# Kernel optimization log

Hardware: AMD Instinct MI355X
Metric: run time of the kernel (lower is better)

The kernel has to match this reference:

```python
import jax, jax.numpy as jnp
import numpy as np

N_NODES = 50000
N_EDGES = 625000
D_FEAT = 128


def setup_inputs() -> dict:
    key = jax.random.key(0)
    k1, k2, k3, k4 = jax.random.split(key, 4)
    h = jax.random.normal(k1, (N_NODES, D_FEAT), dtype=jnp.float32)
    w = jax.random.uniform(k2, (N_EDGES, 1), dtype=jnp.float32)
    src = jax.random.randint(k3, (N_EDGES,), 0, N_NODES, dtype=jnp.int32)
    dst = jax.random.randint(k4, (N_EDGES,), 0, N_NODES, dtype=jnp.int32)
    return {"h": h, "w": w, "src": src, "dst": dst, "mode": 1}


def reference(h, w, src, dst, mode):
    # h: [N, D] node features; w: [E, 1] edge weights; src/dst: [E] edge list.
    n = h.shape[0]
    if mode == 1:  # 'polar': m = h[src] * w, sum to dst  (edge-weighted SpMM)
        msg = h[src] * w  # [E, D]
        out = jax.ops.segment_sum(msg, dst, num_segments=n)
    else:  # GCN symmetric normalization: D^{-1/2} A D^{-1/2} h (out-degree based)
        deg = jax.ops.segment_sum(jnp.ones(src.shape[0], dtype=h.dtype), src,
                                  num_segments=n)
        norm = jnp.power(deg, -0.5)[:, None]  # [N, 1]
        feat = h * norm
        out = jax.ops.segment_sum(feat[src], dst, num_segments=n)
        out = norm * out
    return out
```

## Files before the change

kernel.cpp:

```cpp
#include <hip/hip_runtime.h>
#include <hip/hip_fp16.h>

#define D_FEAT 128


__device__ __forceinline__ unsigned wq16(float f) {
    int q = (int)(f * 65536.0f);
    if (q < 0) q = 0;
    if (q > 65535) q = 65535;
    return (unsigned)q;
}

__device__ __forceinline__ unsigned h2u(__half2 v) {
    union { __half2 h; unsigned u; } cv; cv.h = v; return cv.u;
}
__device__ __forceinline__ float2 u2f2(unsigned u) {
    union { unsigned u; __half2 h; } cv; cv.u = u;
    return __half22float2(cv.h);
}

__global__ void bucket_conv_kernel(const float* __restrict__ h,
                                   const int* __restrict__ src, const int* __restrict__ dst,
                                   const float* __restrict__ w,
                                   int* __restrict__ cursor, float* __restrict__ deg,
                                   int* __restrict__ ovfcnt, int* __restrict__ ovf,
                                   unsigned* __restrict__ rec, int cap,
                                   uint4* __restrict__ h16,
                                   int E, int nBucketBlocks, int nGroups8, int cs,
                                   const int* __restrict__ mode) {
    if ((int)blockIdx.x >= nBucketBlocks) {
        int i = (blockIdx.x - nBucketBlocks) * blockDim.x + threadIdx.x;
        if (i >= nGroups8) return;
        const float4* hf4 = (const float4*)h;
        float4 x = hf4[2 * i];
        float4 y = hf4[2 * i + 1];
        uint4 o;
        o.x = h2u(__float22half2_rn(make_float2(x.x, x.y)));
        o.y = h2u(__float22half2_rn(make_float2(x.z, x.w)));
        o.z = h2u(__float22half2_rn(make_float2(y.x, y.y)));
        o.w = h2u(__float22half2_rn(make_float2(y.z, y.w)));
        h16[i] = o;
        return;
    }
    int e = blockIdx.x * blockDim.x + threadIdx.x;
    if (e >= E) return;
    bool m1 = (*mode == 1);
    int s = src[e];
    int d = dst[e];
    float wv = w[e];
    if (!m1) atomicAdd(&deg[s], 1.0f);
    int pos = atomicAdd(&cursor[(size_t)d * cs], 1);
    unsigned r = ((unsigned)s << 16) | wq16(wv);
    if (pos < cap) rec[(size_t)d * cap + pos] = r;
    else           ovf[atomicAdd(ovfcnt, 1)] = e;
}

__device__ __forceinline__ unsigned bcast_rec(unsigned r0, unsigned r1, int j) {
    unsigned lo = __shfl(r0, j & 31, 32);
    unsigned hi = __shfl(r1, j & 31, 32);
    return (j < 32) ? lo : hi;
}

__global__ void gather4_f16_kernel(const uint2* __restrict__ h16,
                                   const float* __restrict__ hf,
                                   const int* __restrict__ cursor, const float* __restrict__ deg,
                                   const unsigned* __restrict__ rec, int cap,
                                   const int* __restrict__ ovfcnt, const int* __restrict__ ovf,
                                   const int* __restrict__ src, const int* __restrict__ dst,
                                   const float* __restrict__ w,
                                   float* __restrict__ out, int N, int cs,
                                   const int* __restrict__ mode) {
    long long gid = (long long)blockIdx.x * blockDim.x + threadIdx.x;
    int node = (int)(gid >> 5);
    int lane = (int)(gid & 31);
    if (node >= N) return;
    bool m1 = (*mode == 1);
    int cnt = cursor[(size_t)node * cs];
    int inb = cnt < cap ? cnt : cap;
    const unsigned* row = rec + (size_t)node * cap;
    unsigned r0 = (lane < inb) ? row[lane] : 0u;
    unsigned r1 = (lane + 32 < inb) ? row[lane + 32] : 0u;

    float a0 = 0.f, a1 = 0.f, a2 = 0.f, a3 = 0.f;
    float b0 = 0.f, b1 = 0.f, b2 = 0.f, b3 = 0.f;
    float c0 = 0.f, c1 = 0.f, c2 = 0.f, c3 = 0.f;
    float d0 = 0.f, d1 = 0.f, d2 = 0.f, d3 = 0.f;

    int j = 0;
    if (m1) {
        const float Q = 1.52587890625e-05f;
        for (; j + 7 < inb; j += 8) {
            unsigned m0 = bcast_rec(r0, r1, j);
            unsigned m1r = bcast_rec(r0, r1, j + 1);
            unsigned m2r = bcast_rec(r0, r1, j + 2);
            unsigned m3r = bcast_rec(r0, r1, j + 3);
            unsigned m4r = bcast_rec(r0, r1, j + 4);
            unsigned m5r = bcast_rec(r0, r1, j + 5);
            unsigned m6r = bcast_rec(r0, r1, j + 6);
            unsigned m7r = bcast_rec(r0, r1, j + 7);
            uint2 v0 = h16[(size_t)(m0 >> 16) * 32 + lane];
            uint2 v1 = h16[(size_t)(m1r >> 16) * 32 + lane];
            uint2 v2 = h16[(size_t)(m2r >> 16) * 32 + lane];
            uint2 v3 = h16[(size_t)(m3r >> 16) * 32 + lane];
            uint2 v4 = h16[(size_t)(m4r >> 16) * 32 + lane];
            uint2 v5 = h16[(size_t)(m5r >> 16) * 32 + lane];
            uint2 v6 = h16[(size_t)(m6r >> 16) * 32 + lane];
            uint2 v7 = h16[(size_t)(m7r >> 16) * 32 + lane];
            float sc0 = ((float)(m0 & 0xFFFFu) + 0.5f) * Q;
            float sc1 = ((float)(m1r & 0xFFFFu) + 0.5f) * Q;
            float sc2 = ((float)(m2r & 0xFFFFu) + 0.5f) * Q;
            float sc3 = ((float)(m3r & 0xFFFFu) + 0.5f) * Q;
            float sc4 = ((float)(m4r & 0xFFFFu) + 0.5f) * Q;
            float sc5 = ((float)(m5r & 0xFFFFu) + 0.5f) * Q;
            float sc6 = ((float)(m6r & 0xFFFFu) + 0.5f) * Q;
            float sc7 = ((float)(m7r & 0xFFFFu) + 0.5f) * Q;
            float2 f0a = u2f2(v0.x), f0b = u2f2(v0.y);
            float2 f1a = u2f2(v1.x), f1b = u2f2(v1.y);
            float2 f2a = u2f2(v2.x), f2b = u2f2(v2.y);
            float2 f3a = u2f2(v3.x), f3b = u2f2(v3.y);
            float2 f4a = u2f2(v4.x), f4b = u2f2(v4.y);
            float2 f5a = u2f2(v5.x), f5b = u2f2(v5.y);
            float2 f6a = u2f2(v6.x), f6b = u2f2(v6.y);
            float2 f7a = u2f2(v7.x), f7b = u2f2(v7.y);
            a0 += f0a.x * sc0; a1 += f0a.y * sc0; a2 += f0b.x * sc0; a3 += f0b.y * sc0;
            b0 += f1a.x * sc1; b1 += f1a.y * sc1; b2 += f1b.x * sc1; b3 += f1b.y * sc1;
            c0 += f2a.x * sc2; c1 += f2a.y * sc2; c2 += f2b.x * sc2; c3 += f2b.y * sc2;
            d0 += f3a.x * sc3; d1 += f3a.y * sc3; d2 += f3b.x * sc3; d3 += f3b.y * sc3;
            a0 += f4a.x * sc4; a1 += f4a.y * sc4; a2 += f4b.x * sc4; a3 += f4b.y * sc4;
            b0 += f5a.x * sc5; b1 += f5a.y * sc5; b2 += f5b.x * sc5; b3 += f5b.y * sc5;
            c0 += f6a.x * sc6; c1 += f6a.y * sc6; c2 += f6b.x * sc6; c3 += f6b.y * sc6;
            d0 += f7a.x * sc7; d1 += f7a.y * sc7; d2 += f7b.x * sc7; d3 += f7b.y * sc7;
        }
        for (; j + 3 < inb; j += 4) {
            unsigned m0 = bcast_rec(r0, r1, j);
            unsigned m1r = bcast_rec(r0, r1, j + 1);
            unsigned m2r = bcast_rec(r0, r1, j + 2);
            unsigned m3r = bcast_rec(r0, r1, j + 3);
            float sc0 = ((float)(m0 & 0xFFFFu) + 0.5f) * Q;
            float sc1 = ((float)(m1r & 0xFFFFu) + 0.5f) * Q;
            float sc2 = ((float)(m2r & 0xFFFFu) + 0.5f) * Q;
            float sc3 = ((float)(m3r & 0xFFFFu) + 0.5f) * Q;
            uint2 v0 = h16[(size_t)(m0 >> 16) * 32 + lane];
            uint2 v1 = h16[(size_t)(m1r >> 16) * 32 + lane];
            uint2 v2 = h16[(size_t)(m2r >> 16) * 32 + lane];
            uint2 v3 = h16[(size_t)(m3r >> 16) * 32 + lane];
            float2 f0a = u2f2(v0.x), f0b = u2f2(v0.y);
            float2 f1a = u2f2(v1.x), f1b = u2f2(v1.y);
            float2 f2a = u2f2(v2.x), f2b = u2f2(v2.y);
            float2 f3a = u2f2(v3.x), f3b = u2f2(v3.y);
            a0 += f0a.x * sc0; a1 += f0a.y * sc0; a2 += f0b.x * sc0; a3 += f0b.y * sc0;
            b0 += f1a.x * sc1; b1 += f1a.y * sc1; b2 += f1b.x * sc1; b3 += f1b.y * sc1;
            c0 += f2a.x * sc2; c1 += f2a.y * sc2; c2 += f2b.x * sc2; c3 += f2b.y * sc2;
            d0 += f3a.x * sc3; d1 += f3a.y * sc3; d2 += f3b.x * sc3; d3 += f3b.y * sc3;
        }
        for (; j < inb; ++j) {
            unsigned m0 = bcast_rec(r0, r1, j);
            float sc0 = ((float)(m0 & 0xFFFFu) + 0.5f) * Q;
            uint2 v0 = h16[(size_t)(m0 >> 16) * 32 + lane];
            float2 f0a = u2f2(v0.x), f0b = u2f2(v0.y);
            a0 += f0a.x * sc0; a1 += f0a.y * sc0; a2 += f0b.x * sc0; a3 += f0b.y * sc0;
        }
    } else {
        for (; j + 3 < inb; j += 4) {
            unsigned m0 = bcast_rec(r0, r1, j);
            unsigned m1r = bcast_rec(r0, r1, j + 1);
            unsigned m2r = bcast_rec(r0, r1, j + 2);
            unsigned m3r = bcast_rec(r0, r1, j + 3);
            int s0 = (int)(m0 >> 16), s1 = (int)(m1r >> 16);
            int s2 = (int)(m2r >> 16), s3 = (int)(m3r >> 16);
            float sc0 = rsqrtf(deg[s0]);
            float sc1 = rsqrtf(deg[s1]);
            float sc2 = rsqrtf(deg[s2]);
            float sc3 = rsqrtf(deg[s3]);
            uint2 v0 = h16[(size_t)s0 * 32 + lane];
            uint2 v1 = h16[(size_t)s1 * 32 + lane];
            uint2 v2 = h16[(size_t)s2 * 32 + lane];
            uint2 v3 = h16[(size_t)s3 * 32 + lane];
            float2 f0a = u2f2(v0.x), f0b = u2f2(v0.y);
            float2 f1a = u2f2(v1.x), f1b = u2f2(v1.y);
            float2 f2a = u2f2(v2.x), f2b = u2f2(v2.y);
            float2 f3a = u2f2(v3.x), f3b = u2f2(v3.y);
            a0 += f0a.x * sc0; a1 += f0a.y * sc0; a2 += f0b.x * sc0; a3 += f0b.y * sc0;
            b0 += f1a.x * sc1; b1 += f1a.y * sc1; b2 += f1b.x * sc1; b3 += f1b.y * sc1;
            c0 += f2a.x * sc2; c1 += f2a.y * sc2; c2 += f2b.x * sc2; c3 += f2b.y * sc2;
            d0 += f3a.x * sc3; d1 += f3a.y * sc3; d2 += f3b.x * sc3; d3 += f3b.y * sc3;
        }
        for (; j < inb; ++j) {
            unsigned m0 = bcast_rec(r0, r1, j);
            int s0 = (int)(m0 >> 16);
            float sc0 = rsqrtf(deg[s0]);
            uint2 v0 = h16[(size_t)s0 * 32 + lane];
            float2 f0a = u2f2(v0.x), f0b = u2f2(v0.y);
            a0 += f0a.x * sc0; a1 += f0a.y * sc0; a2 += f0b.x * sc0; a3 += f0b.y * sc0;
        }
    }

    a0 += b0 + c0 + d0; a1 += b1 + c1 + d1;
    a2 += b2 + c2 + d2; a3 += b3 + c3 + d3;

    if (cnt > cap) {
        int total = *ovfcnt;
        for (int k = 0; k < total; ++k) {
            int e = ovf[k];
            if (dst[e] == node) {
                int s = src[e];
                float sc = m1 ? w[e] : rsqrtf(deg[s]);
                float4 v = ((const float4*)(hf + (long long)s * D_FEAT))[lane];
                a0 += v.x * sc; a1 += v.y * sc; a2 += v.z * sc; a3 += v.w * sc;
            }
        }
    }
    float fin = m1 ? 1.0f : rsqrtf(deg[node]);
    float4 r; r.x = a0 * fin; r.y = a1 * fin; r.z = a2 * fin; r.w = a3 * fin;
    ((float4*)(out + (long long)node * D_FEAT))[lane] = r;
}


__global__ void bucket_multi_kernel(const int* __restrict__ src, const int* __restrict__ dst,
                                    const float* __restrict__ w,
                                    int* __restrict__ cursor, float* __restrict__ deg,
                                    int* __restrict__ ovfcnt, int* __restrict__ ovf,
                                    unsigned* __restrict__ rec, int cap,
                                    int E, const int* __restrict__ mode) {
    int e = blockIdx.x * blockDim.x + threadIdx.x;
    if (e >= E) return;
    bool m1 = (*mode == 1);
    int s = src[e], d = dst[e];
    if (!m1) atomicAdd(&deg[s], 1.0f);
    int pos = atomicAdd(&cursor[d], 1);
    if (pos < cap) rec[(size_t)d * cap + pos] = ((unsigned)s << 16) | wq16(w[e]);
    else ovf[atomicAdd(ovfcnt, 1)] = e;
}

__global__ void gather4_f32_kernel(const float* __restrict__ h,
                                   const int* __restrict__ cursor, const float* __restrict__ deg,
                                   const unsigned* __restrict__ rec, int cap,
                                   const int* __restrict__ ovfcnt, const int* __restrict__ ovf,
                                   const int* __restrict__ src, const int* __restrict__ dst,
                                   const float* __restrict__ w,
                                   float* __restrict__ out, int N, const int* __restrict__ mode) {
    long long gid = (long long)blockIdx.x * blockDim.x + threadIdx.x;
    int node = (int)(gid >> 5);
    int lane = (int)(gid & 31);
    if (node >= N) return;
    bool m1 = (*mode == 1);
    int cnt = cursor[node];
    int inb = cnt < cap ? cnt : cap;
    const unsigned* row = rec + (size_t)node * cap;
    unsigned r0 = (lane < inb) ? row[lane] : 0u;
    unsigned r1 = (lane + 32 < inb) ? row[lane + 32] : 0u;
    const float4* h4 = (const float4*)h;
    float a0 = 0.f, a1 = 0.f, a2 = 0.f, a3 = 0.f;
    float b0 = 0.f, b1 = 0.f, b2 = 0.f, b3 = 0.f;
    int j = 0;
    const float Q = 1.52587890625e-05f;
    for (; j + 1 < inb; j += 2) {
        unsigned m0 = bcast_rec(r0, r1, j);
        unsigned m1r = bcast_rec(r0, r1, j + 1);
        int s0 = (int)(m0 >> 16), s1 = (int)(m1r >> 16);
        float sc0 = m1 ? ((float)(m0 & 0xFFFFu) + 0.5f) * Q : rsqrtf(deg[s0]);
        float sc1 = m1 ? ((float)(m1r & 0xFFFFu) + 0.5f) * Q : rsqrtf(deg[s1]);
        float4 v0 = h4[(size_t)s0 * 32 + lane];
        float4 v1 = h4[(size_t)s1 * 32 + lane];
        a0 += v0.x * sc0; a1 += v0.y * sc0; a2 += v0.z * sc0; a3 += v0.w * sc0;
        b0 += v1.x * sc1; b1 += v1.y * sc1; b2 += v1.z * sc1; b3 += v1.w * sc1;
    }
    if (j < inb) {
        unsigned m0 = bcast_rec(r0, r1, j);
        int s0 = (int)(m0 >> 16);
        float sc0 = m1 ? ((float)(m0 & 0xFFFFu) + 0.5f) * Q : rsqrtf(deg[s0]);
        float4 v0 = h4[(size_t)s0 * 32 + lane];
        a0 += v0.x * sc0; a1 += v0.y * sc0; a2 += v0.z * sc0; a3 += v0.w * sc0;
    }
    a0 += b0; a1 += b1; a2 += b2; a3 += b3;
    if (cnt > cap) {
        int total = *ovfcnt;
        for (int k = 0; k < total; ++k) {
            int e = ovf[k];
            if (dst[e] == node) {
                int s = src[e];
                float sc = m1 ? w[e] : rsqrtf(deg[s]);
                float4 v = ((const float4*)(h + (long long)s * D_FEAT))[lane];
                a0 += v.x * sc; a1 += v.y * sc; a2 += v.z * sc; a3 += v.w * sc;
            }
        }
    }
    float fin = m1 ? 1.0f : rsqrtf(deg[node]);
    float4 r; r.x = a0 * fin; r.y = a1 * fin; r.z = a2 * fin; r.w = a3 * fin;
    ((float4*)(out + (long long)node * D_FEAT))[lane] = r;
}


__global__ void fb_deg_kernel(const int* __restrict__ src, float* __restrict__ deg,
                              int E, const int* __restrict__ mode) {
    if (*mode == 1) return;
    int e = blockIdx.x * blockDim.x + threadIdx.x;
    if (e < E) atomicAdd(&deg[src[e]], 1.0f);
}
__global__ void fb_norm_kernel(const float* __restrict__ deg, float* __restrict__ norm,
                               int N, const int* __restrict__ mode) {
    if (*mode == 1) return;
    int i = blockIdx.x * blockDim.x + threadIdx.x;
    if (i < N) norm[i] = rsqrtf(deg[i]);
}
__global__ void fb_scatter_kernel(const float* __restrict__ h, const float* __restrict__ w,
                                  const int* __restrict__ src, const int* __restrict__ dst,
                                  const float* __restrict__ norm, float* __restrict__ out,
                                  int E, const int* __restrict__ mode) {
    long long gid = (long long)blockIdx.x * blockDim.x + threadIdx.x;
    int e = (int)(gid >> 5);
    int lane = (int)(gid & 31);
    if (e >= E) return;
    int s = src[e], d = dst[e];
    float scale = (*mode == 1) ? w[e] : norm[s];
    float4 v = ((const float4*)(h + (long long)s * D_FEAT))[lane];
    float* op = out + (long long)d * D_FEAT + lane * 4;
    atomicAdd(op + 0, v.x * scale);
    atomicAdd(op + 1, v.y * scale);
    atomicAdd(op + 2, v.z * scale);
    atomicAdd(op + 3, v.w * scale);
}
__global__ void fb_scale_kernel(float* __restrict__ out, const float* __restrict__ norm,
                                int N, const int* __restrict__ mode) {
    if (*mode == 1) return;
    int idx = blockIdx.x * blockDim.x + threadIdx.x;
    int total = N * (D_FEAT / 4);
    if (idx >= total) return;
    int node = idx / (D_FEAT / 4);
    float4* op = (float4*)out + idx;
    float4 v = *op;
    float nn = norm[node];
    v.x *= nn; v.y *= nn; v.z *= nn; v.w *= nn;
    *op = v;
}


extern "C" void kernel_launch(void* const* d_in, const int* in_sizes, int n_in,
                              void* d_out, int out_size, void* d_ws, size_t ws_size,
                              hipStream_t stream) {
    const float* h    = (const float*)d_in[0];
    const float* w    = (const float*)d_in[1];
    const int*   src  = (const int*)d_in[2];
    const int*   dst  = (const int*)d_in[3];
    const int*   mode = (const int*)d_in[4];

    int ND = in_sizes[0];
    int E  = in_sizes[1];
    int N  = ND / D_FEAT;

    float* out = (float*)d_out;

    size_t ws_words = ws_size / 4;

    for (int cs : {16, 4, 1}) {
        size_t cur_words   = (size_t)N * cs;
        size_t fixed_words = cur_words + (size_t)N + 1 + (size_t)E;
        size_t h16_off     = (fixed_words + 3) & ~(size_t)3;
        size_t h16_words   = (size_t)N * (D_FEAT / 2);
        size_t rec16_off   = h16_off + h16_words;
        long capH = 0;
        if (ws_words > rec16_off) capH = (long)((ws_words - rec16_off) / (size_t)N);
        if (capH > 64) capH = 64;

        if (N <= 65536 && capH >= 28) {
            int*      cursor = (int*)d_ws;
            float*    deg    = (float*)(cursor + cur_words);
            int*      ovfcnt = (int*)(deg + N);
            int*      ovf    = ovfcnt + 1;
            uint4*    h16    = (uint4*)((int*)d_ws + h16_off);
            unsigned* rec    = (unsigned*)((int*)d_ws + rec16_off);
            int cap = (int)capH;
            int csv = cs;
            size_t zero_words = cur_words + (size_t)N + 1;

            hipMemsetAsync(d_ws, 0, zero_words * sizeof(int), stream);

            int nGroups8    = ND / 8;
            int nBucketBlks = (E + 255) / 256;
            int nConvBlks   = (nGroups8 + 255) / 256;
            bucket_conv_kernel<<<nBucketBlks + nConvBlks, 256, 0, stream>>>(
                h, src, dst, w, cursor, deg, ovfcnt, ovf, rec, cap, h16,
                E, nBucketBlks, nGroups8, csv, mode);

            long long gt = (long long)N * 32;
            gather4_f16_kernel<<<(int)((gt + 255) / 256), 256, 0, stream>>>(
                (const uint2*)h16, h, cursor, deg, rec, cap, ovfcnt, ovf, src, dst, w,
                out, N, csv, mode);
            return;
        }
    }

    size_t fixed_words = 2 * (size_t)N + 1 + (size_t)E;
    int*   cursor = (int*)d_ws;
    float* deg    = (float*)(cursor + N);
    int*   ovfcnt = (int*)(deg + N);
    int*   ovf    = ovfcnt + 1;

    size_t rec_off = fixed_words;
    long capA = 0;
    if (ws_words > rec_off) capA = (long)((ws_words - rec_off) / (size_t)N);
    if (capA > 64) capA = 64;

    if (N <= 65536 && capA >= 28) {
        unsigned* rec = (unsigned*)((int*)d_ws + rec_off);
        int cap = (int)capA;
        hipMemsetAsync(d_ws, 0, (2 * (size_t)N + 1) * sizeof(int), stream);
        bucket_multi_kernel<<<(E + 255) / 256, 256, 0, stream>>>(
            src, dst, w, cursor, deg, ovfcnt, ovf, rec, cap, E, mode);
        long long gt = (long long)N * 32;
        gather4_f32_kernel<<<(int)((gt + 255) / 256), 256, 0, stream>>>(
            h, cursor, deg, rec, cap, ovfcnt, ovf, src, dst, w, out, N, mode);
        return;
    }

    float* degF  = (float*)d_ws;
    float* normF = degF + N;
    hipMemsetAsync(d_out, 0, (size_t)out_size * sizeof(float), stream);
    hipMemsetAsync(d_ws, 0, (size_t)N * sizeof(float), stream);
    fb_deg_kernel<<<(E + 255) / 256, 256, 0, stream>>>(src, degF, E, mode);
    fb_norm_kernel<<<(N + 255) / 256, 256, 0, stream>>>(degF, normF, N, mode);
    long long tt = (long long)E * 32;
    fb_scatter_kernel<<<(int)((tt + 255) / 256), 256, 0, stream>>>(h, w, src, dst,
                                                                   normF, out, E, mode);
    int st = N * (D_FEAT / 4);
    fb_scale_kernel<<<(st + 255) / 256, 256, 0, stream>>>(out, normF, N, mode);
}
```

Before: 154.1 us.

## Split per-node bucket cursor into four sub-cursors to cut atomic contention

The bucketing step now spreads each destination's atomic cursor across four padded sub-counters, chosen by edge index mod 4, each owning a quarter of the record capacity. The gather kernel reads the four counts and maps a flat edge index to a segment position with a small branchy helper. The aim is to reduce same-address atomic contention during bucketing. In exchange it adds a larger zeroed cursor region (64 words per node), per-edge index arithmetic in the gather loop, loss of the 8-wide unrolled loop, and a higher chance of overflow because each quarter bucket can fill on its own.

```diff
diff --git a/kernel.cpp b/kernel.cpp
--- a/kernel.cpp
+++ b/kernel.cpp
@@ -24,9 +24,9 @@
                                    const float* __restrict__ w,
                                    int* __restrict__ cursor, float* __restrict__ deg,
                                    int* __restrict__ ovfcnt, int* __restrict__ ovf,
-                                   unsigned* __restrict__ rec, int cap,
+                                   unsigned* __restrict__ rec, int cap, int capq,
                                    uint4* __restrict__ h16,
-                                   int E, int nBucketBlocks, int nGroups8, int cs,
+                                   int E, int nBucketBlocks, int nGroups8,
                                    const int* __restrict__ mode) {
     if ((int)blockIdx.x >= nBucketBlocks) {
         int i = (blockIdx.x - nBucketBlocks) * blockDim.x + threadIdx.x;
@@ -49,10 +49,11 @@
     int d = dst[e];
     float wv = w[e];
     if (!m1) atomicAdd(&deg[s], 1.0f);
-    int pos = atomicAdd(&cursor[(size_t)d * cs], 1);
+    int kq = e & 3;
+    int pos = atomicAdd(&cursor[(size_t)d * 64 + kq * 16], 1);
     unsigned r = ((unsigned)s << 16) | wq16(wv);
-    if (pos < cap) rec[(size_t)d * cap + pos] = r;
-    else           ovf[atomicAdd(ovfcnt, 1)] = e;
+    if (pos < capq) rec[(size_t)d * cap + kq * capq + pos] = r;
+    else            ovf[atomicAdd(ovfcnt, 1)] = e;
 }
 
 __device__ __forceinline__ unsigned bcast_rec(unsigned r0, unsigned r1, int j) {
@@ -61,81 +62,61 @@
     return (j < 32) ? lo : hi;
 }
 
+__device__ __forceinline__ int segidx(int t, int c0, int c1, int c2, int capq) {
+    if (t < c0) return t;
+    t -= c0;
+    if (t < c1) return capq + t;
+    t -= c1;
+    if (t < c2) return 2 * capq + t;
+    t -= c2;
+    return 3 * capq + t;
+}
+
 __global__ void gather4_f16_kernel(const uint2* __restrict__ h16,
                                    const float* __restrict__ hf,
                                    const int* __restrict__ cursor, const float* __restrict__ deg,
-                                   const unsigned* __restrict__ rec, int cap,
+                                   const unsigned* __restrict__ rec, int cap, int capq,
                                    const int* __restrict__ ovfcnt, const int* __restrict__ ovf,
                                    const int* __restrict__ src, const int* __restrict__ dst,
                                    const float* __restrict__ w,
-                                   float* __restrict__ out, int N, int cs,
+                                   float* __restrict__ out, int N,
                                    const int* __restrict__ mode) {
     long long gid = (long long)blockIdx.x * blockDim.x + threadIdx.x;
     int node = (int)(gid >> 5);
     int lane = (int)(gid & 31);
     if (node >= N) return;
     bool m1 = (*mode == 1);
-    int cnt = cursor[(size_t)node * cs];
-    int inb = cnt < cap ? cnt : cap;
+
+    const int* cbase = cursor + (size_t)node * 64;
+    int n0 = cbase[0], n1 = cbase[16], n2 = cbase[32], n3 = cbase[48];
+    int c0 = n0 < capq ? n0 : capq;
+    int c1 = n1 < capq ? n1 : capq;
+    int c2 = n2 < capq ? n2 : capq;
+    int c3 = n3 < capq ? n3 : capq;
+    int total = c0 + c1 + c2 + c3;
+    bool ovfl = (n0 > capq) | (n1 > capq) | (n2 > capq) | (n3 > capq);
+
     const unsigned* row = rec + (size_t)node * cap;
-    unsigned r0 = (lane < inb) ? row[lane] : 0u;
-    unsigned r1 = (lane + 32 < inb) ? row[lane + 32] : 0u;
+    unsigned r0 = (lane < cap) ? row[lane] : 0u;
+    unsigned r1 = (lane + 32 < cap) ? row[lane + 32] : 0u;
 
     float a0 = 0.f, a1 = 0.f, a2 = 0.f, a3 = 0.f;
     float b0 = 0.f, b1 = 0.f, b2 = 0.f, b3 = 0.f;
-    float c0 = 0.f, c1 = 0.f, c2 = 0.f, c3 = 0.f;
+    float e0 = 0.f, e1 = 0.f, e2 = 0.f, e3 = 0.f;
     float d0 = 0.f, d1 = 0.f, d2 = 0.f, d3 = 0.f;
 
-    int j = 0;
+    int t = 0;
     if (m1) {
         const float Q = 1.52587890625e-05f;
-        for (; j + 7 < inb; j += 8) {
-            unsigned m0 = bcast_rec(r0, r1, j);
-            unsigned m1r = bcast_rec(r0, r1, j + 1);
-            unsigned m2r = bcast_rec(r0, r1, j + 2);
-            unsigned m3r = bcast_rec(r0, r1, j + 3);
-            unsigned m4r = bcast_rec(r0, r1, j + 4);
-            unsigned m5r = bcast_rec(r0, r1, j + 5);
-            unsigned m6r = bcast_rec(r0, r1, j + 6);
-            unsigned m7r = bcast_rec(r0, r1, j + 7);
-            uint2 v0 = h16[(size_t)(m0 >> 16) * 32 + lane];
-            uint2 v1 = h16[(size_t)(m1r >> 16) * 32 + lane];
-            uint2 v2 = h16[(size_t)(m2r >> 16) * 32 + lane];
-            uint2 v3 = h16[(size_t)(m3r >> 16) * 32 + lane];
-            uint2 v4 = h16[(size_t)(m4r >> 16) * 32 + lane];
-            uint2 v5 = h16[(size_t)(m5r >> 16) * 32 + lane];
-            uint2 v6 = h16[(size_t)(m6r >> 16) * 32 + lane];
-            uint2 v7 = h16[(size_t)(m7r >> 16) * 32 + lane];
-            float sc0 = ((float)(m0 & 0xFFFFu) + 0.5f) * Q;
-            float sc1 = ((float)(m1r & 0xFFFFu) + 0.5f) * Q;
-            float sc2 = ((float)(m2r & 0xFFFFu) + 0.5f) * Q;
-            float sc3 = ((float)(m3r & 0xFFFFu) + 0.5f) * Q;
-            float sc4 = ((float)(m4r & 0xFFFFu) + 0.5f) * Q;
-            float sc5 = ((float)(m5r & 0xFFFFu) + 0.5f) * Q;
-            float sc6 = ((float)(m6r & 0xFFFFu) + 0.5f) * Q;
-            float sc7 = ((float)(m7r & 0xFFFFu) + 0.5f) * Q;
-            float2 f0a = u2f2(v0.x), f0b = u2f2(v0.y);
-            float2 f1a = u2f2(v1.x), f1b = u2f2(v1.y);
-            float2 f2a = u2f2(v2.x), f2b = u2f2(v2.y);
-            float2 f3a = u2f2(v3.x), f3b = u2f2(v3.y);
-            float2 f4a = u2f2(v4.x), f4b = u2f2(v4.y);
-            float2 f5a = u2f2(v5.x), f5b = u2f2(v5.y);
-            float2 f6a = u2f2(v6.x), f6b = u2f2(v6.y);
-            float2 f7a = u2f2(v7.x), f7b = u2f2(v7.y);
-            a0 += f0a.x * sc0; a1 += f0a.y * sc0; a2 += f0b.x * sc0; a3 += f0b.y * sc0;
-            b0 += f1a.x * sc1; b1 += f1a.y * sc1; b2 += f1b.x * sc1; b3 += f1b.y * sc1;
-            c0 += f2a.x * sc2; c1 += f2a.y * sc2; c2 += f2b.x * sc2; c3 += f2b.y * sc2;
-            d0 += f3a.x * sc3; d1 += f3a.y * sc3; d2 += f3b.x * sc3; d3 += f3b.y * sc3;
-            a0 += f4a.x * sc4; a1 += f4a.y * sc4; a2 += f4b.x * sc4; a3 += f4b.y * sc4;
-            b0 += f5a.x * sc5; b1 += f5a.y * sc5; b2 += f5b.x * sc5; b3 += f5b.y * sc5;
-            c0 += f6a.x * sc6; c1 += f6a.y * sc6; c2 += f6b.x * sc6; c3 += f6b.y * sc6;
-            d0 += f7a.x * sc7; d1 += f7a.y * sc7; d2 += f7b.x * sc7; d3 += f7b.y * sc7;
-        }
-        for (; j + 3 < inb; j += 4) {
-            unsigned m0 = bcast_rec(r0, r1, j);
-            unsigned m1r = bcast_rec(r0, r1, j + 1);
-            unsigned m2r = bcast_rec(r0, r1, j + 2);
-            unsigned m3r = bcast_rec(r0, r1, j + 3);
+        for (; t + 3 < total; t += 4) {
+            int i0 = segidx(t,     c0, c1, c2, capq);
+            int i1 = segidx(t + 1, c0, c1, c2, capq);
+            int i2 = segidx(t + 2, c0, c1, c2, capq);
+            int i3 = segidx(t + 3, c0, c1, c2, capq);
+            unsigned m0 = bcast_rec(r0, r1, i0);
+            unsigned m1r = bcast_rec(r0, r1, i1);
+            unsigned m2r = bcast_rec(r0, r1, i2);
+            unsigned m3r = bcast_rec(r0, r1, i3);
             float sc0 = ((float)(m0 & 0xFFFFu) + 0.5f) * Q;
             float sc1 = ((float)(m1r & 0xFFFFu) + 0.5f) * Q;
             float sc2 = ((float)(m2r & 0xFFFFu) + 0.5f) * Q;
@@ -150,22 +131,27 @@
             float2 f3a = u2f2(v3.x), f3b = u2f2(v3.y);
             a0 += f0a.x * sc0; a1 += f0a.y * sc0; a2 += f0b.x * sc0; a3 += f0b.y * sc0;
             b0 += f1a.x * sc1; b1 += f1a.y * sc1; b2 += f1b.x * sc1; b3 += f1b.y * sc1;
-            c0 += f2a.x * sc2; c1 += f2a.y * sc2; c2 += f2b.x * sc2; c3 += f2b.y * sc2;
+            e0 += f2a.x * sc2; e1 += f2a.y * sc2; e2 += f2b.x * sc2; e3 += f2b.y * sc2;
             d0 += f3a.x * sc3; d1 += f3a.y * sc3; d2 += f3b.x * sc3; d3 += f3b.y * sc3;
         }
-        for (; j < inb; ++j) {
-            unsigned m0 = bcast_rec(r0, r1, j);
+        for (; t < total; ++t) {
+            int i0 = segidx(t, c0, c1, c2, capq);
+            unsigned m0 = bcast_rec(r0, r1, i0);
             float sc0 = ((float)(m0 & 0xFFFFu) + 0.5f) * Q;
             uint2 v0 = h16[(size_t)(m0 >> 16) * 32 + lane];
             float2 f0a = u2f2(v0.x), f0b = u2f2(v0.y);
             a0 += f0a.x * sc0; a1 += f0a.y * sc0; a2 += f0b.x * sc0; a3 += f0b.y * sc0;
         }
     } else {
-        for (; j + 3 < inb; j += 4) {
-            unsigned m0 = bcast_rec(r0, r1, j);
-            unsigned m1r = bcast_rec(r0, r1, j + 1);
-            unsigned m2r = bcast_rec(r0, r1, j + 2);
-            unsigned m3r = bcast_rec(r0, r1, j + 3);
+        for (; t + 3 < total; t += 4) {
+            int i0 = segidx(t,     c0, c1, c2, capq);
+            int i1 = segidx(t + 1, c0, c1, c2, capq);
+            int i2 = segidx(t + 2, c0, c1, c2, capq);
+            int i3 = segidx(t + 3, c0, c1, c2, capq);
+            unsigned m0 = bcast_rec(r0, r1, i0);
+            unsigned m1r = bcast_rec(r0, r1, i1);
+            unsigned m2r = bcast_rec(r0, r1, i2);
+            unsigned m3r = bcast_rec(r0, r1, i3);
             int s0 = (int)(m0 >> 16), s1 = (int)(m1r >> 16);
             int s2 = (int)(m2r >> 16), s3 = (int)(m3r >> 16);
             float sc0 = rsqrtf(deg[s0]);
@@ -182,11 +168,12 @@
             float2 f3a = u2f2(v3.x), f3b = u2f2(v3.y);
             a0 += f0a.x * sc0; a1 += f0a.y * sc0; a2 += f0b.x * sc0; a3 += f0b.y * sc0;
             b0 += f1a.x * sc1; b1 += f1a.y * sc1; b2 += f1b.x * sc1; b3 += f1b.y * sc1;
-            c0 += f2a.x * sc2; c1 += f2a.y * sc2; c2 += f2b.x * sc2; c3 += f2b.y * sc2;
+            e0 += f2a.x * sc2; e1 += f2a.y * sc2; e2 += f2b.x * sc2; e3 += f2b.y * sc2;
             d0 += f3a.x * sc3; d1 += f3a.y * sc3; d2 += f3b.x * sc3; d3 += f3b.y * sc3;
         }
-        for (; j < inb; ++j) {
-            unsigned m0 = bcast_rec(r0, r1, j);
+        for (; t < total; ++t) {
+            int i0 = segidx(t, c0, c1, c2, capq);
+            unsigned m0 = bcast_rec(r0, r1, i0);
             int s0 = (int)(m0 >> 16);
             float sc0 = rsqrtf(deg[s0]);
             uint2 v0 = h16[(size_t)s0 * 32 + lane];
@@ -195,12 +182,12 @@
         }
     }
 
-    a0 += b0 + c0 + d0; a1 += b1 + c1 + d1;
-    a2 += b2 + c2 + d2; a3 += b3 + c3 + d3;
-
-    if (cnt > cap) {
-        int total = *ovfcnt;
-        for (int k = 0; k < total; ++k) {
+    a0 += b0 + e0 + d0; a1 += b1 + e1 + d1;
+    a2 += b2 + e2 + d2; a3 += b3 + e3 + d3;
+
+    if (ovfl) {
+        int tot = *ovfcnt;
+        for (int k = 0; k < tot; ++k) {
             int e = ovf[k];
             if (dst[e] == node) {
                 int s = src[e];
@@ -352,8 +339,8 @@
 
     size_t ws_words = ws_size / 4;
 
-    for (int cs : {16, 4, 1}) {
-        size_t cur_words   = (size_t)N * cs;
+    {
+        size_t cur_words   = (size_t)N * 64;
         size_t fixed_words = cur_words + (size_t)N + 1 + (size_t)E;
         size_t h16_off     = (fixed_words + 3) & ~(size_t)3;
         size_t h16_words   = (size_t)N * (D_FEAT / 2);
@@ -361,16 +348,17 @@
         long capH = 0;
         if (ws_words > rec16_off) capH = (long)((ws_words - rec16_off) / (size_t)N);
         if (capH > 64) capH = 64;
-
-        if (N <= 65536 && capH >= 28) {
+        capH &= ~3L;
+
+        if (N <= 65536 && capH >= 32) {
             int*      cursor = (int*)d_ws;
             float*    deg    = (float*)(cursor + cur_words);
             int*      ovfcnt = (int*)(deg + N);
             int*      ovf    = ovfcnt + 1;
             uint4*    h16    = (uint4*)((int*)d_ws + h16_off);
             unsigned* rec    = (unsigned*)((int*)d_ws + rec16_off);
-            int cap = (int)capH;
-            int csv = cs;
+            int cap  = (int)capH;
+            int capq = cap / 4;
             size_t zero_words = cur_words + (size_t)N + 1;
 
             hipMemsetAsync(d_ws, 0, zero_words * sizeof(int), stream);
@@ -379,13 +367,13 @@
             int nBucketBlks = (E + 255) / 256;
             int nConvBlks   = (nGroups8 + 255) / 256;
             bucket_conv_kernel<<<nBucketBlks + nConvBlks, 256, 0, stream>>>(
-                h, src, dst, w, cursor, deg, ovfcnt, ovf, rec, cap, h16,
-                E, nBucketBlks, nGroups8, csv, mode);
+                h, src, dst, w, cursor, deg, ovfcnt, ovf, rec, cap, capq, h16,
+                E, nBucketBlks, nGroups8, mode);
 
             long long gt = (long long)N * 32;
             gather4_f16_kernel<<<(int)((gt + 255) / 256), 256, 0, stream>>>(
-                (const uint2*)h16, h, cursor, deg, rec, cap, ovfcnt, ovf, src, dst, w,
-                out, N, csv, mode);
+                (const uint2*)h16, h, cursor, deg, rec, cap, capq, ovfcnt, ovf,
+                src, dst, w, out, N, mode);
             return;
         }
     }
```

Result: no change. 155.6 us (+1.0%).
